# Performance work log

Hardware: AMD Instinct MI355X
Metric: run time of the kernel (lower is better)

The kernel has to match this reference:

```python
import jax, jax.numpy as jnp
import numpy as np
import math

B, N = 64, 16384
POS_IN, HID, DIR_IN = 63, 128, 27
COLOR_IN = HID + DIR_IN  # 155
POS_W, POS_B = POS_IN * HID, HID          # 8064, 128
SIG_W, SIG_B = HID * 1, 1                  # 128, 1
COL_W, COL_B = COLOR_IN * 3, 3             # 465... actually 155*3=465? no: 465
TOTAL = POS_W + POS_B + SIG_W + SIG_B + COL_W + COL_B  # 8717


def pos_encode(x, num_freqs):
    # x: [..., 3] -> [..., 3 + 2*3*num_freqs], order: x, (sin f0, cos f0, sin f1, cos f1, ...)
    freqs = (2.0 ** jnp.arange(num_freqs, dtype=x.dtype)) * math.pi  # [L]
    xb = x[..., None, :] * freqs[:, None]                            # [..., L, 3]
    sc = jnp.stack([jnp.sin(xb), jnp.cos(xb)], axis=-2)              # [..., L, 2, 3]
    sc = sc.reshape(*x.shape[:-1], num_freqs * 2 * x.shape[-1])
    return jnp.concatenate([x, sc], axis=-1)


def setup_inputs() -> dict:
    key = jax.random.key(0)
    k1, k2, k3 = jax.random.split(key, 3)
    positions = jax.random.normal(k1, (B, N, 3), dtype=jnp.float32)
    directions = jax.random.normal(k2, (B, N, 3), dtype=jnp.float32)
    params = jax.random.normal(k3, (B, TOTAL), dtype=jnp.float32) * 0.1
    return {"positions": positions, "directions": directions, "params": params}


def reference(positions, directions, params):
    pos_enc = pos_encode(positions, 10)   # [B, N, 63]
    dir_enc = pos_encode(directions, 4)   # [B, N, 27]

    i = 0
    pw = params[:, i:i + POS_W].reshape(B, HID, POS_IN); i += POS_W
    pb = params[:, i:i + POS_B]; i += POS_B
    sw = params[:, i:i + SIG_W].reshape(B, 1, HID); i += SIG_W
    sb = params[:, i:i + SIG_B]; i += SIG_B
    cw = params[:, i:i + COL_W].reshape(B, 3, COLOR_IN); i += COL_W
    cb = params[:, i:i + COL_B]

    h = jnp.einsum('bnd,bhd->bnh', pos_enc, pw) + pb[:, None, :]
    h = jax.nn.relu(h)                                   # [B, N, 128]
    sigma = jnp.einsum('bnh,boh->bno', h, sw) + sb[:, None, :]  # [B, N, 1]
    h_dir = jnp.concatenate([h, dir_enc], axis=-1)       # [B, N, 155]
    rgb = jnp.einsum('bnc,boc->bno', h_dir, cw) + cb[:, None, :]
    rgb = jax.nn.sigmoid(rgb)                            # [B, N, 3]
    return sigma, rgb
```

## Files before the change

### kernel.cpp

```cpp
#include <hip/hip_runtime.h>
#include <hip/hip_bf16.h>


#define NB 64
#define NRAY 16384
#define NTOTAL 8789
#define PI_F 3.14159265358979323846f

typedef short bf16x8 __attribute__((ext_vector_type(8)));
typedef float f32x16 __attribute__((ext_vector_type(16)));

union U8 { unsigned u[4]; bf16x8 v; };

__device__ __forceinline__ unsigned pk2(float a, float b) {
    float2 t; t.x = a; t.y = b;
    __hip_bfloat162 h = __float22bfloat162_rn(t);
    return *reinterpret_cast<unsigned*>(&h);
}

__global__ __launch_bounds__(256, 2) void nerf_mfma_kernel(
    const float* __restrict__ pos,
    const float* __restrict__ dir,
    const float* __restrict__ params,
    float* __restrict__ out)
{
    const int tid  = threadIdx.x;
    const int lane = tid & 63;
    const int wid  = tid >> 6;
    const int hi   = lane >> 5;
    const int l31  = lane & 31;

    const int b     = blockIdx.x >> 4;
    const int chunk = (blockIdx.x & 15) << 10;
    const float* __restrict__ p = params + b * NTOTAL;

    __shared__ uint4 encs[2048];
    char* encb = reinterpret_cast<char*>(encs);

    bf16x8 aw[4][4];
    #pragma unroll
    for (int mt = 0; mt < 4; ++mt) {
        const int hrow = mt * 32 + l31;
        const float* wrow = p + hrow * 63;
        const float bias = p[8064 + hrow];
        #pragma unroll
        for (int ks = 0; ks < 4; ++ks) {
            U8 u;
            #pragma unroll
            for (int j = 0; j < 4; ++j) {
                const int k0 = ks * 16 + hi * 8 + 2 * j;
                const int k1 = k0 + 1;
                const float e0 = (k0 < 3) ? wrow[k0] : (k0 == 3 ? bias : wrow[k0 - 1]);
                const float e1 = (k1 < 3) ? wrow[k1] : (k1 == 3 ? bias : wrow[k1 - 1]);
                u.u[j] = pk2(e0, e1);
            }
            aw[mt][ks] = u.v;
        }
    }
    bf16x8 haw[8];
    {
        const int r = l31 & 3;
        const float* w2 = (r == 0) ? (p + 8192) : (p + 8321 + (r - 1) * 155);
        #pragma unroll
        for (int s = 0; s < 8; ++s) {
            const int base = 32 * (s >> 1) + 16 * (s & 1) + 4 * hi;
            U8 u;
            #pragma unroll
            for (int j = 0; j < 4; ++j) {
                const int i0 = 2 * j, i1 = 2 * j + 1;
                u.u[j] = pk2(w2[base + (i0 & 3) + 8 * (i0 >> 2)],
                             w2[base + (i1 & 3) + 8 * (i1 >> 2)]);
            }
            haw[s] = u.v;
        }
    }

    f32x16 FZ;
    #pragma unroll
    for (int i = 0; i < 16; ++i) FZ[i] = 0.f;

    const float sb  = p[8320];
    const float cb0 = p[8786], cb1 = p[8787], cb2 = p[8788];
    const float* __restrict__ cwr  = p + 8321 + 128;
    const float* __restrict__ cwg  = p + 8321 + 155 + 128;
    const float* __restrict__ cwb2 = p + 8321 + 310 + 128;

    const int rayBlock = b * NRAY + chunk;
    float* __restrict__ rgbout = out + (long)NB * NRAY;
    const long pb0 = (long)(rayBlock + tid) * 3;

    auto encode_row = [&](const float3 Pv) {
        const int swz = (tid & 7) << 4;
        char* myrow = encb + tid * 128;
        float s0, c0, s1, c1, s2, c2;
        __sincosf(Pv.x * PI_F, &s0, &c0);
        __sincosf(Pv.y * PI_F, &s1, &c1);
        __sincosf(Pv.z * PI_F, &s2, &c2);
        unsigned w[32];
        w[0] = pk2(Pv.x, Pv.y);
        w[1] = pk2(Pv.z, 1.0f);
        #pragma unroll
        for (int f = 0; f < 10; ++f) {
            w[2 + 3 * f] = pk2(s0, s1);
            w[3 + 3 * f] = pk2(s2, c0);
            w[4 + 3 * f] = pk2(c1, c2);
            if (f < 9) {
                float t;
                t = 2.f * s0 * c0; c0 = fmaf(-2.f * s0, s0, 1.f); s0 = t;
                t = 2.f * s1 * c1; c1 = fmaf(-2.f * s1, s1, 1.f); s1 = t;
                t = 2.f * s2 * c2; c2 = fmaf(-2.f * s2, s2, 1.f); s2 = t;
            }
        }
        #pragma unroll
        for (int cq = 0; cq < 8; ++cq) {
            uint4 v;
            v.x = w[4 * cq + 0]; v.y = w[4 * cq + 1];
            v.z = w[4 * cq + 2]; v.w = w[4 * cq + 3];
            *reinterpret_cast<uint4*>(myrow + ((cq * 16) ^ swz)) = v;
        }
    };

    float3 P0 = *reinterpret_cast<const float3*>(pos + pb0);
    float3 Pn = *reinterpret_cast<const float3*>(pos + pb0 + 768);
    float3 Dc = *reinterpret_cast<const float3*>(dir + pb0);
    encode_row(P0);

    #pragma unroll 1
    for (int it = 0; it < 4; ++it) {
        const int ray = rayBlock + it * 256 + tid;

        float3 Pn2, Dn;
        if (it < 2) Pn2 = *reinterpret_cast<const float3*>(pos + pb0 + (it + 2) * 768);
        if (it < 3) Dn  = *reinterpret_cast<const float3*>(dir + pb0 + (it + 1) * 768);

        bf16x8 be[2][4];
        #pragma unroll
        for (int nt = 0; nt < 2; ++nt) {
            const int row = wid * 64 + nt * 32 + l31;
            const int swz = (row & 7) << 4;
            #pragma unroll
            for (int ks = 0; ks < 4; ++ks)
                be[nt][ks] = *reinterpret_cast<const bf16x8*>(
                    encb + row * 128 + ((ks * 32 + hi * 16) ^ swz));
        }

        if (it < 3) encode_row(Pn);

        __builtin_amdgcn_s_setprio(1);
        float hres[2][4];
        #pragma unroll
        for (int nt = 0; nt < 2; ++nt) {
            f32x16 hacc;
            #pragma unroll
            for (int mt = 0; mt < 4; ++mt) {
                f32x16 accm = __builtin_amdgcn_mfma_f32_32x32x16_bf16(aw[mt][0], be[nt][0], FZ, 0, 0, 0);
                accm = __builtin_amdgcn_mfma_f32_32x32x16_bf16(aw[mt][1], be[nt][1], accm, 0, 0, 0);
                accm = __builtin_amdgcn_mfma_f32_32x32x16_bf16(aw[mt][2], be[nt][2], accm, 0, 0, 0);
                accm = __builtin_amdgcn_mfma_f32_32x32x16_bf16(aw[mt][3], be[nt][3], accm, 0, 0, 0);

                #pragma unroll
                for (int t = 0; t < 2; ++t) {
                    const int rb = t * 8;
                    U8 u;
                    #pragma unroll
                    for (int j = 0; j < 4; ++j)
                        u.u[j] = pk2(fmaxf(accm[rb + 2 * j], 0.f),
                                     fmaxf(accm[rb + 2 * j + 1], 0.f));
                    hacc = __builtin_amdgcn_mfma_f32_32x32x16_bf16(
                        haw[2 * mt + t], u.v, (mt == 0 && t == 0) ? FZ : hacc, 0, 0, 0);
                }
            }
            hres[nt][0] = hacc[0]; hres[nt][1] = hacc[1];
            hres[nt][2] = hacc[2]; hres[nt][3] = hacc[3];
        }
        __builtin_amdgcn_s_setprio(0);

        const float hv0 = hi ? hres[1][0] : hres[0][0];
        const float hv1 = hi ? hres[1][1] : hres[0][1];
        const float hv2 = hi ? hres[1][2] : hres[0][2];
        const float hv3 = hi ? hres[1][3] : hres[0][3];

        float sig = hv0 + sb;
        float cr  = hv1 + cb0;
        float cg  = hv2 + cb1;
        float cbl = hv3 + cb2;

        {
            float s0, c0, s1, c1, s2, c2;
            __sincosf(Dc.x * PI_F, &s0, &c0);
            __sincosf(Dc.y * PI_F, &s1, &c1);
            __sincosf(Dc.z * PI_F, &s2, &c2);
            cr  = fmaf(Dc.x, cwr[0], cr);  cg  = fmaf(Dc.x, cwg[0], cg);  cbl = fmaf(Dc.x, cwb2[0], cbl);
            cr  = fmaf(Dc.y, cwr[1], cr);  cg  = fmaf(Dc.y, cwg[1], cg);  cbl = fmaf(Dc.y, cwb2[1], cbl);
            cr  = fmaf(Dc.z, cwr[2], cr);  cg  = fmaf(Dc.z, cwg[2], cg);  cbl = fmaf(Dc.z, cwb2[2], cbl);
            #pragma unroll
            for (int f = 0; f < 4; ++f) {
                const int j = 3 + 6 * f;
                cr = fmaf(s0, cwr[j+0], cr); cg = fmaf(s0, cwg[j+0], cg); cbl = fmaf(s0, cwb2[j+0], cbl);
                cr = fmaf(s1, cwr[j+1], cr); cg = fmaf(s1, cwg[j+1], cg); cbl = fmaf(s1, cwb2[j+1], cbl);
                cr = fmaf(s2, cwr[j+2], cr); cg = fmaf(s2, cwg[j+2], cg); cbl = fmaf(s2, cwb2[j+2], cbl);
                cr = fmaf(c0, cwr[j+3], cr); cg = fmaf(c0, cwg[j+3], cg); cbl = fmaf(c0, cwb2[j+3], cbl);
                cr = fmaf(c1, cwr[j+4], cr); cg = fmaf(c1, cwg[j+4], cg); cbl = fmaf(c1, cwb2[j+4], cbl);
                cr = fmaf(c2, cwr[j+5], cr); cg = fmaf(c2, cwg[j+5], cg); cbl = fmaf(c2, cwb2[j+5], cbl);
                if (f < 3) {
                    float t;
                    t = 2.f * s0 * c0; c0 = fmaf(-2.f * s0, s0, 1.f); s0 = t;
                    t = 2.f * s1 * c1; c1 = fmaf(-2.f * s1, s1, 1.f); s1 = t;
                    t = 2.f * s2 * c2; c2 = fmaf(-2.f * s2, s2, 1.f); s2 = t;
                }
            }
        }

        cr  = 1.0f / (1.0f + __expf(-cr));
        cg  = 1.0f / (1.0f + __expf(-cg));
        cbl = 1.0f / (1.0f + __expf(-cbl));

        out[ray] = sig;
        float3 rgbv; rgbv.x = cr; rgbv.y = cg; rgbv.z = cbl;
        *reinterpret_cast<float3*>(rgbout + (long)ray * 3) = rgbv;

        Pn = Pn2; Dc = Dn;
    }
}

extern "C" void kernel_launch(void* const* d_in, const int* in_sizes, int n_in,
                              void* d_out, int out_size, void* d_ws, size_t ws_size,
                              hipStream_t stream) {
    const float* pos    = (const float*)d_in[0];
    const float* dirs   = (const float*)d_in[1];
    const float* params = (const float*)d_in[2];
    float* out = (float*)d_out;

    dim3 grid(1024);
    dim3 block(256);
    nerf_mfma_kernel<<<grid, block, 0, stream>>>(pos, dirs, params, out);
}
```

Measured before the change: 53.83 us.

## Stage color-head weights in LDS and halve rays per block for occupancy

```diff
diff --git a/kernel.cpp b/kernel.cpp
--- a/kernel.cpp
+++ b/kernel.cpp
@@ -18,7 +18,7 @@
     return *reinterpret_cast<unsigned*>(&h);
 }
 
-__global__ __launch_bounds__(256, 2) void nerf_mfma_kernel(
+__global__ __launch_bounds__(256, 3) void nerf_mfma_kernel(
     const float* __restrict__ pos,
     const float* __restrict__ dir,
     const float* __restrict__ params,
@@ -30,12 +30,29 @@
     const int hi   = lane >> 5;
     const int l31  = lane & 31;
 
-    const int b     = blockIdx.x >> 4;
-    const int chunk = (blockIdx.x & 15) << 10;
+    const int b     = blockIdx.x >> 5;
+    const int chunk = (blockIdx.x & 31) << 9;
     const float* __restrict__ p = params + b * NTOTAL;
 
     __shared__ uint4 encs[2048];
+    __shared__ unsigned hawLds[8 * 2 * 4 * 4];
     char* encb = reinterpret_cast<char*>(encs);
+    const char* hawb = reinterpret_cast<const char*>(hawLds);
+
+    if (tid < 64) {
+        const int s  = tid & 7;
+        const int hh = (tid >> 3) & 1;
+        const int r  = tid >> 4;
+        const float* w2 = (r == 0) ? (p + 8192) : (p + 8321 + (r - 1) * 155);
+        const int base = 32 * (s >> 1) + 16 * (s & 1) + 4 * hh;
+        unsigned* dst = &hawLds[(((s << 1) + hh) * 4 + r) * 4];
+        #pragma unroll
+        for (int j = 0; j < 4; ++j) {
+            const int i0 = 2 * j, i1 = 2 * j + 1;
+            dst[j] = pk2(w2[base + (i0 & 3) + 8 * (i0 >> 2)],
+                         w2[base + (i1 & 3) + 8 * (i1 >> 2)]);
+        }
+    }
 
     bf16x8 aw[4][4];
     #pragma unroll
@@ -57,23 +74,6 @@
             aw[mt][ks] = u.v;
         }
     }
-    bf16x8 haw[8];
-    {
-        const int r = l31 & 3;
-        const float* w2 = (r == 0) ? (p + 8192) : (p + 8321 + (r - 1) * 155);
-        #pragma unroll
-        for (int s = 0; s < 8; ++s) {
-            const int base = 32 * (s >> 1) + 16 * (s & 1) + 4 * hi;
-            U8 u;
-            #pragma unroll
-            for (int j = 0; j < 4; ++j) {
-                const int i0 = 2 * j, i1 = 2 * j + 1;
-                u.u[j] = pk2(w2[base + (i0 & 3) + 8 * (i0 >> 2)],
-                             w2[base + (i1 & 3) + 8 * (i1 >> 2)]);
-            }
-            haw[s] = u.v;
-        }
-    }
 
     f32x16 FZ;
     #pragma unroll
@@ -88,6 +88,7 @@
     const int rayBlock = b * NRAY + chunk;
     float* __restrict__ rgbout = out + (long)NB * NRAY;
     const long pb0 = (long)(rayBlock + tid) * 3;
+    const int hoff = hi * 64 + (l31 & 3) * 16;
 
     auto encode_row = [&](const float3 Pv) {
         const int swz = (tid & 7) << 4;
@@ -96,14 +97,27 @@
         __sincosf(Pv.x * PI_F, &s0, &c0);
         __sincosf(Pv.y * PI_F, &s1, &c1);
         __sincosf(Pv.z * PI_F, &s2, &c2);
-        unsigned w[32];
-        w[0] = pk2(Pv.x, Pv.y);
-        w[1] = pk2(Pv.z, 1.0f);
+        unsigned wb[4];
+        wb[0] = pk2(Pv.x, Pv.y);
+        wb[1] = pk2(Pv.z, 1.0f);
         #pragma unroll
         for (int f = 0; f < 10; ++f) {
-            w[2 + 3 * f] = pk2(s0, s1);
-            w[3 + 3 * f] = pk2(s2, c0);
-            w[4 + 3 * f] = pk2(c1, c2);
+            const int w = 2 + 3 * f;
+            wb[(w + 0) & 3] = pk2(s0, s1);
+            if (((w + 0) & 3) == 3) {
+                uint4 v; v.x = wb[0]; v.y = wb[1]; v.z = wb[2]; v.w = wb[3];
+                *reinterpret_cast<uint4*>(myrow + ((((w + 0) >> 2) * 16) ^ swz)) = v;
+            }
+            wb[(w + 1) & 3] = pk2(s2, c0);
+            if (((w + 1) & 3) == 3) {
+                uint4 v; v.x = wb[0]; v.y = wb[1]; v.z = wb[2]; v.w = wb[3];
+                *reinterpret_cast<uint4*>(myrow + ((((w + 1) >> 2) * 16) ^ swz)) = v;
+            }
+            wb[(w + 2) & 3] = pk2(c1, c2);
+            if (((w + 2) & 3) == 3) {
+                uint4 v; v.x = wb[0]; v.y = wb[1]; v.z = wb[2]; v.w = wb[3];
+                *reinterpret_cast<uint4*>(myrow + ((((w + 2) >> 2) * 16) ^ swz)) = v;
+            }
             if (f < 9) {
                 float t;
                 t = 2.f * s0 * c0; c0 = fmaf(-2.f * s0, s0, 1.f); s0 = t;
@@ -111,27 +125,18 @@
                 t = 2.f * s2 * c2; c2 = fmaf(-2.f * s2, s2, 1.f); s2 = t;
             }
         }
-        #pragma unroll
-        for (int cq = 0; cq < 8; ++cq) {
-            uint4 v;
-            v.x = w[4 * cq + 0]; v.y = w[4 * cq + 1];
-            v.z = w[4 * cq + 2]; v.w = w[4 * cq + 3];
-            *reinterpret_cast<uint4*>(myrow + ((cq * 16) ^ swz)) = v;
-        }
     };
 
-    float3 P0 = *reinterpret_cast<const float3*>(pos + pb0);
+    float3 Pc = *reinterpret_cast<const float3*>(pos + pb0);
     float3 Pn = *reinterpret_cast<const float3*>(pos + pb0 + 768);
     float3 Dc = *reinterpret_cast<const float3*>(dir + pb0);
-    encode_row(P0);
+    float3 Dn = *reinterpret_cast<const float3*>(dir + pb0 + 768);
+    encode_row(Pc);
+    __syncthreads();
 
     #pragma unroll 1
-    for (int it = 0; it < 4; ++it) {
+    for (int it = 0; it < 2; ++it) {
         const int ray = rayBlock + it * 256 + tid;
-
-        float3 Pn2, Dn;
-        if (it < 2) Pn2 = *reinterpret_cast<const float3*>(pos + pb0 + (it + 2) * 768);
-        if (it < 3) Dn  = *reinterpret_cast<const float3*>(dir + pb0 + (it + 1) * 768);
 
         bf16x8 be[2][4];
         #pragma unroll
@@ -144,7 +149,7 @@
                     encb + row * 128 + ((ks * 32 + hi * 16) ^ swz));
         }
 
-        if (it < 3) encode_row(Pn);
+        if (it < 1) encode_row(Pn);
 
         __builtin_amdgcn_s_setprio(1);
         float hres[2][4];
@@ -166,8 +171,11 @@
                     for (int j = 0; j < 4; ++j)
                         u.u[j] = pk2(fmaxf(accm[rb + 2 * j], 0.f),
                                      fmaxf(accm[rb + 2 * j + 1], 0.f));
+                    const int s = 2 * mt + t;
+                    const bf16x8 hw = *reinterpret_cast<const bf16x8*>(
+                        hawb + s * 128 + hoff);
                     hacc = __builtin_amdgcn_mfma_f32_32x32x16_bf16(
-                        haw[2 * mt + t], u.v, (mt == 0 && t == 0) ? FZ : hacc, 0, 0, 0);
+                        hw, u.v, (s == 0) ? FZ : hacc, 0, 0, 0);
                 }
             }
             hres[nt][0] = hacc[0]; hres[nt][1] = hacc[1];
@@ -219,7 +227,7 @@
         float3 rgbv; rgbv.x = cr; rgbv.y = cg; rgbv.z = cbl;
         *reinterpret_cast<float3*>(rgbout + (long)ray * 3) = rgbv;
 
-        Pn = Pn2; Dc = Dn;
+        Dc = Dn;
     }
 }
 
@@ -231,7 +239,7 @@
     const float* params = (const float*)d_in[2];
     float* out = (float*)d_out;
 
-    dim3 grid(1024);
+    dim3 grid(NB * 32);
     dim3 block(256);
     nerf_mfma_kernel<<<grid, block, 0, stream>>>(pos, dirs, params, out);
 }
```

New measurement: 90.22 us. 1.68x slower.
